# Kernel optimization log

Hardware: AMD Instinct MI355X
Metric: run time of the kernel (lower is better)

The kernel has to match this reference:

```python
import jax, jax.numpy as jnp
import numpy as np

B, S, HID = 2, 2048, 2048
H, KVH, D = 32, 4, 128
EPS = 1e-6
ROPE_THETA = 1e6
INIT = 0.02


def setup_inputs() -> dict:
    key = jax.random.key(0)
    ks = jax.random.split(key, 6)
    hidden_states = jax.random.normal(ks[0], (B, S, HID), jnp.float32)
    q_w = jax.random.normal(ks[1], (HID, H * D), jnp.float32) * INIT
    k_w = jax.random.normal(ks[2], (HID, KVH * D), jnp.float32) * INIT
    v_w = jax.random.normal(ks[3], (HID, KVH * D), jnp.float32) * INIT
    o_w = jax.random.normal(ks[4], (H * D, HID), jnp.float32) * INIT
    q_norm_w = jnp.ones((D,), jnp.float32)
    k_norm_w = jnp.ones((D,), jnp.float32)
    # rotary embeddings, computed once per position (B, S, D)
    pos = jnp.arange(S, dtype=jnp.float32)
    inv_freq = 1.0 / (ROPE_THETA ** (jnp.arange(0, D, 2, dtype=jnp.float32) / D))
    freqs = pos[:, None] * inv_freq[None, :]          # (S, D/2)
    emb = jnp.concatenate([freqs, freqs], axis=-1)    # (S, D)
    cos = jnp.broadcast_to(jnp.cos(emb)[None], (B, S, D))
    sin = jnp.broadcast_to(jnp.sin(emb)[None], (B, S, D))
    # causal mask (is_causal=True, sliding_window=None)
    attn_mask = jnp.tril(jnp.ones((S, S), bool))[None, None]  # (1,1,S,S)
    return {"hidden_states": hidden_states, "cos": cos, "sin": sin,
            "q_w": q_w, "k_w": k_w, "v_w": v_w, "o_w": o_w,
            "q_norm_w": q_norm_w, "k_norm_w": k_norm_w, "attn_mask": attn_mask}


def _rms_norm(x, w):
    xf = x.astype(jnp.float32)
    var = jnp.mean(jax.lax.square(xf), axis=-1, keepdims=True)
    return (w * (xf * jax.lax.rsqrt(var + EPS))).astype(x.dtype)


def _rotate_half(x):
    x1, x2 = jnp.split(x, 2, axis=-1)
    return jnp.concatenate([-x2, x1], axis=-1)


def _apply_rope(q, k, cos, sin):
    # q: (B,H,S,D), k: (B,KVH,S,D); cos/sin: (B,S,D) -> (B,1,S,D)
    cos = cos[:, None]
    sin = sin[:, None]
    q = q * cos + _rotate_half(q) * sin
    k = k * cos + _rotate_half(k) * sin
    return q, k


def reference(hidden_states, cos, sin, q_w, k_w, v_w, o_w, q_norm_w, k_norm_w, attn_mask):
    b, s, _ = hidden_states.shape
    scaling = D ** (-0.5)
    # projections + per-head QK RMSNorm
    q = _rms_norm((hidden_states @ q_w).reshape(b, s, H, D), q_norm_w)
    k = _rms_norm((hidden_states @ k_w).reshape(b, s, KVH, D), k_norm_w)
    v = (hidden_states @ v_w).reshape(b, s, KVH, D)
    q = jnp.transpose(q, (0, 2, 1, 3))   # (b,H,s,D)
    k = jnp.transpose(k, (0, 2, 1, 3))   # (b,KVH,s,D)
    v = jnp.transpose(v, (0, 2, 1, 3))
    q, k = _apply_rope(q, k, cos, sin)
    # GQA: repeat KV heads across groups
    groups = H // KVH
    k = jnp.repeat(k, groups, axis=1)    # (b,H,s,D)
    v = jnp.repeat(v, groups, axis=1)
    # eager softmax attention (fp32 softmax)
    scores = jnp.einsum('bhqd,bhkd->bhqk', q, k).astype(jnp.float32) * scaling
    scores = jnp.where(attn_mask, scores, jnp.float32(-1e30))
    probs = jax.nn.softmax(scores, axis=-1).astype(q.dtype)
    attn = jnp.einsum('bhqk,bhkd->bhqd', probs, v)
    attn = jnp.transpose(attn, (0, 2, 1, 3)).reshape(b, s, H * D)
    return attn @ o_w
```

## Files before the change

kernel.cpp:

```cpp
#include <hip/hip_runtime.h>
#include <hip/hip_bf16.h>

typedef unsigned short u16;
typedef __attribute__((ext_vector_type(4))) float f32x4;
typedef __attribute__((ext_vector_type(16))) float f32x16;
typedef __attribute__((ext_vector_type(8))) short bf16x8;
typedef __attribute__((ext_vector_type(4))) unsigned u32x4;

#define B_ 2
#define S_ 2048
#define HID_ 2048
#define H_ 32
#define KVH_ 4
#define D_ 128
#define M_ 4096
#define NQ_ 4096
#define NKV_ 512

typedef const __attribute__((address_space(1))) void gconst_void;
typedef __attribute__((address_space(3))) void lds_void;

static __device__ __forceinline__ void gload_lds16(const void* g, void* l) {
  __builtin_amdgcn_global_load_lds((gconst_void*)g, (lds_void*)l, 16, 0, 0);
}

#define WAITV(N) asm volatile("s_waitcnt vmcnt(" #N ")" ::: "memory")
#define WAITL0() asm volatile("s_waitcnt lgkmcnt(0)" ::: "memory")
#define SBAR() __builtin_amdgcn_s_barrier()
#define SCHED0() __builtin_amdgcn_sched_barrier(0)
#define CFENCE() asm volatile("" ::: "memory")

static __device__ __forceinline__ u16 f2b(float f) {
  union { float f; unsigned i; } x; x.f = f;
  return (u16)((x.i + 0x7fffu + ((x.i >> 16) & 1u)) >> 16);
}
static __device__ __forceinline__ float b2f(u16 u) {
  union { unsigned i; float f; } x; x.i = ((unsigned)u) << 16;
  return x.f;
}
static __device__ __forceinline__ float max3f(float a, float b, float c) {
  float d;
  asm("v_max3_f32 %0, %1, %2, %3" : "=v"(d) : "v"(a), "v"(b), "v"(c));
  return d;
}

static __device__ __forceinline__ void tr_tile(const float* __restrict__ W,
    u16* __restrict__ Wt, int K, int N, int n0, int k0, u16 (*t)[72]) {
  int tid = threadIdx.x;
  int r = tid >> 4;
  int c4 = (tid & 15) * 4;
#pragma unroll
  for (int i = 0; i < 4; i++) {
    int k = r + i * 16;
    float4 v = *reinterpret_cast<const float4*>(W + (size_t)(k0 + k) * N + n0 + c4);
    t[k][c4 + 0] = f2b(v.x); t[k][c4 + 1] = f2b(v.y);
    t[k][c4 + 2] = f2b(v.z); t[k][c4 + 3] = f2b(v.w);
  }
  __syncthreads();
#pragma unroll
  for (int i = 0; i < 4; i++) {
    int n = r + i * 16;
    ushort4 o;
    o.x = t[c4 + 0][n]; o.y = t[c4 + 1][n]; o.z = t[c4 + 2][n]; o.w = t[c4 + 3][n];
    *reinterpret_cast<ushort4*>(Wt + (size_t)(n0 + n) * K + k0 + c4) = o;
  }
}

__global__ __launch_bounds__(256) void k_prep(const float* __restrict__ hidden, u16* __restrict__ hb,
    const float* __restrict__ qw, u16* __restrict__ qwt,
    const float* __restrict__ kw, u16* __restrict__ kwt,
    const float* __restrict__ vw, u16* __restrict__ vwt,
    const float* __restrict__ ow, u16* __restrict__ owt) {
  __shared__ u16 t[64][72];
  const int bid = blockIdx.x;
  if (bid < 2048) {
    const int n4 = M_ * HID_ / 4;
    int i = bid * 256 + threadIdx.x;
    const int stride = 2048 * 256;
    for (; i < n4; i += stride) {
      float4 v = reinterpret_cast<const float4*>(hidden)[i];
      ushort4 o;
      o.x = f2b(v.x); o.y = f2b(v.y); o.z = f2b(v.z); o.w = f2b(v.w);
      reinterpret_cast<ushort4*>(hb)[i] = o;
    }
  } else if (bid < 4096) {
    int l = bid - 2048;
    tr_tile(qw, qwt, HID_, NQ_, (l & 63) * 64, (l >> 6) * 64, t);
  } else if (bid < 4352) {
    int l = bid - 4096;
    tr_tile(kw, kwt, HID_, NKV_, (l & 7) * 64, (l >> 3) * 64, t);
  } else if (bid < 4608) {
    int l = bid - 4352;
    tr_tile(vw, vwt, HID_, NKV_, (l & 7) * 64, (l >> 3) * 64, t);
  } else {
    int l = bid - 4608;
    tr_tile(ow, owt, NQ_, HID_, (l & 31) * 64, (l >> 5) * 64, t);
  }
}

__device__ __forceinline__ void gemm_core(const u16* __restrict__ A, const u16* __restrict__ Bt,
                                          int K, int m0, int n0,
                                          u16* As, u16* Bs, f32x4 (&acc)[4][4]) {
  const int tid = threadIdx.x;
  const int lane = tid & 63;
  const int wid = tid >> 6;
  const int wr = wid >> 1, wc = wid & 1;
  const int lrow = lane & 15;
  const int hi = lane >> 4;
  const f32x4 zz = {0.f, 0.f, 0.f, 0.f};
#pragma unroll
  for (int i = 0; i < 4; i++)
#pragma unroll
    for (int j = 0; j < 4; j++) acc[i][j] = zz;

  const int srow = tid >> 3;
  const int sc16 = tid & 7;
  const int nk = K >> 6;
  int cur = 0;

#pragma unroll
  for (int rep = 0; rep < 4; rep++) {
    int row = rep * 32 + srow;
    int gcol = ((sc16 ^ (row & 7)) << 3);
    gload_lds16(A + (size_t)(m0 + row) * K + gcol, As + row * 64 + sc16 * 8);
    gload_lds16(Bt + (size_t)(n0 + row) * K + gcol, Bs + row * 64 + sc16 * 8);
  }

  for (int t = 0; t < nk; t++) {
    if (t + 1 < nk) {
      int nxt = cur ^ 1;
      int kb = (t + 1) << 6;
#pragma unroll
      for (int rep = 0; rep < 4; rep++) {
        int row = rep * 32 + srow;
        int gcol = kb + ((sc16 ^ (row & 7)) << 3);
        gload_lds16(A + (size_t)(m0 + row) * K + gcol, As + nxt * 8192 + row * 64 + sc16 * 8);
        gload_lds16(Bt + (size_t)(n0 + row) * K + gcol, Bs + nxt * 8192 + row * 64 + sc16 * 8);
      }
      WAITV(8);
    } else {
      WAITV(0);
    }
    SCHED0(); SBAR(); CFENCE(); SCHED0();

    const u16* Ac = As + cur * 8192;
    const u16* Bc = Bs + cur * 8192;
#pragma unroll
    for (int kc = 0; kc < 2; kc++) {
      bf16x8 af[4], bfr[4];
#pragma unroll
      for (int i = 0; i < 4; i++) {
        int row = wr * 64 + i * 16 + lrow;
        af[i] = *reinterpret_cast<const bf16x8*>(Ac + row * 64 + ((((kc << 2) + hi) ^ (row & 7)) << 3));
      }
#pragma unroll
      for (int j = 0; j < 4; j++) {
        int row = wc * 64 + j * 16 + lrow;
        bfr[j] = *reinterpret_cast<const bf16x8*>(Bc + row * 64 + ((((kc << 2) + hi) ^ (row & 7)) << 3));
      }
#pragma unroll
      for (int i = 0; i < 4; i++)
#pragma unroll
        for (int j = 0; j < 4; j++)
          acc[i][j] = __builtin_amdgcn_mfma_f32_16x16x32_bf16(af[i], bfr[j], acc[i][j], 0, 0, 0);
    }
    SBAR(); SCHED0();
    cur ^= 1;
  }
}

__global__ __launch_bounds__(512, 2) void k_gemm_q8(const u16* __restrict__ A,
    const u16* __restrict__ Bt, u16* __restrict__ qb) {
  __shared__ u16 Ash[2][2][128 * 64];
  __shared__ u16 Bsh[2][2][128 * 64];
  const int bid = blockIdx.x;
  const int wg = (bid & 7) * 32 + (bid >> 3);
  const int mt = wg & 15, nt = wg >> 4;
  const int m0 = mt * 256, n0 = nt * 256;
  const int K = HID_, nk = K >> 6;
  const int tid = threadIdx.x, lane = tid & 63;
  const int wv = tid >> 6, wr = wv >> 2, wc = wv & 3;
  const int lrow = lane & 15, hi4 = lane >> 4;

  const int s0r = tid >> 3, sc = tid & 7;
  const int s1r = (tid + 512) >> 3;

  auto stgA = [&](int h, int t, int d) {
    gload_lds16(A + (size_t)(m0 + h * 128 + s0r) * K + t * 64 + ((sc ^ (s0r & 7)) << 3),
                &Ash[d][h][s0r * 64 + sc * 8]);
    gload_lds16(A + (size_t)(m0 + h * 128 + s1r) * K + t * 64 + ((sc ^ (s1r & 7)) << 3),
                &Ash[d][h][s1r * 64 + sc * 8]);
  };
  auto stgB = [&](int h, int t, int d) {
    gload_lds16(Bt + (size_t)(n0 + h * 128 + s0r) * K + t * 64 + ((sc ^ (s0r & 7)) << 3),
                &Bsh[d][h][s0r * 64 + sc * 8]);
    gload_lds16(Bt + (size_t)(n0 + h * 128 + s1r) * K + t * 64 + ((sc ^ (s1r & 7)) << 3),
                &Bsh[d][h][s1r * 64 + sc * 8]);
  };

  f32x4 acc[8][4];
  const f32x4 zz = {0.f, 0.f, 0.f, 0.f};
#pragma unroll
  for (int f = 0; f < 8; f++)
#pragma unroll
    for (int j = 0; j < 4; j++) acc[f][j] = zz;

  bf16x8 af0[4][2], af1[4][2], bfr[2][2];

  auto lda = [&](bf16x8 (&dst)[4][2], int mh, int d) {
#pragma unroll
    for (int fi = 0; fi < 4; fi++) {
      int row = fi * 32 + wr * 16 + lrow;
#pragma unroll
      for (int kk = 0; kk < 2; kk++)
        dst[fi][kk] = *reinterpret_cast<const bf16x8*>(
            &Ash[d][mh][row * 64 + ((((kk << 2) + hi4) ^ (row & 7)) << 3)]);
    }
  };
  auto ldb = [&](int nh, int d) {
#pragma unroll
    for (int ji = 0; ji < 2; ji++) {
      int row = ji * 64 + wc * 16 + lrow;
#pragma unroll
      for (int kk = 0; kk < 2; kk++)
        bfr[ji][kk] = *reinterpret_cast<const bf16x8*>(
            &Bsh[d][nh][row * 64 + ((((kk << 2) + hi4) ^ (row & 7)) << 3)]);
    }
  };
  auto mq = [&](bf16x8 (&afh)[4][2], int mh, int nh) {
    __builtin_amdgcn_s_setprio(1);
#pragma unroll
    for (int kk = 0; kk < 2; kk++)
#pragma unroll
      for (int fi = 0; fi < 4; fi++)
#pragma unroll
        for (int ji = 0; ji < 2; ji++)
          acc[mh * 4 + fi][nh * 2 + ji] = __builtin_amdgcn_mfma_f32_16x16x32_bf16(
              afh[fi][kk], bfr[ji][kk], acc[mh * 4 + fi][nh * 2 + ji], 0, 0, 0);
    __builtin_amdgcn_s_setprio(0);
  };

  stgA(0, 0, 0); stgA(1, 0, 0); stgB(0, 0, 0); stgB(1, 0, 0);
  WAITV(2); SCHED0();
  SBAR(); SCHED0();

  for (int t = 0; t < nk; t++) {
    const int d = t & 1, nd = d ^ 1;
    const bool pre = (t + 1 < nk);
    lda(af0, 0, d); ldb(0, d);
    if (pre) stgA(0, t + 1, nd);
    SCHED0(); SBAR();
    WAITL0(); SCHED0();
    mq(af0, 0, 0);
    SBAR(); SCHED0();
    lda(af1, 1, d);
    if (pre) stgA(1, t + 1, nd);
    WAITV(4); SCHED0(); SBAR();
    WAITL0(); SCHED0();
    mq(af1, 1, 0);
    SBAR(); SCHED0();
    ldb(1, d);
    if (pre) stgB(0, t + 1, nd);
    SCHED0(); SBAR();
    WAITL0(); SCHED0();
    mq(af1, 1, 1);
    SBAR(); SCHED0();
    if (pre) stgB(1, t + 1, nd);
    WAITV(2); SCHED0(); SBAR();
    mq(af0, 0, 1);
    SBAR(); SCHED0();
  }

  const int lr4 = hi4 * 4, lc = lane & 15;
#pragma unroll
  for (int f = 0; f < 8; f++)
#pragma unroll
    for (int j = 0; j < 4; j++)
#pragma unroll
      for (int rr = 0; rr < 4; rr++) {
        int m = m0 + f * 32 + wr * 16 + lr4 + rr;
        int ncol = n0 + j * 64 + wc * 16 + lc;
        int b = m >> 11, s = m & (S_ - 1);
        int head = ncol >> 7, dd = ncol & 127;
        qb[(((size_t)b * H_ + head) * S_ + s) * D_ + dd] = f2b(acc[f][j][rr]);
      }
}

__global__ __launch_bounds__(256, 2) void k_gemm_kv(const u16* __restrict__ hb,
    const u16* __restrict__ kwt, const u16* __restrict__ vwt,
    u16* __restrict__ kb, u16* __restrict__ vb) {
  __shared__ u16 As[2 * 128 * 64], Bs[2 * 128 * 64];
  const int bid = blockIdx.x;
  const int wg = (bid & 7) * 32 + (bid >> 3);
  const int mt = wg & 31, nt = wg >> 5;
  const bool isv = nt >= 4;
  const int head = isv ? nt - 4 : nt;
  const u16* Bt = isv ? vwt : kwt;
  f32x4 acc[4][4];
  gemm_core(hb, Bt, HID_, mt * 128, head * 128, As, Bs, acc);
  const int lane = threadIdx.x & 63;
  const int wid = threadIdx.x >> 6;
  const int wr = wid >> 1, wc = wid & 1;
  const int lr4 = (lane >> 4) * 4, lc = lane & 15;
#pragma unroll
  for (int i = 0; i < 4; i++)
#pragma unroll
    for (int j = 0; j < 4; j++)
#pragma unroll
      for (int r = 0; r < 4; r++) {
        int m = mt * 128 + wr * 64 + i * 16 + lr4 + r;
        int d = wc * 64 + j * 16 + lc;
        int b = m >> 11, s = m & (S_ - 1);
        u16 val = f2b(acc[i][j][r]);
        if (isv) vb[(((size_t)b * KVH_ + head) * D_ + d) * S_ + s] = val;
        else     kb[(((size_t)b * KVH_ + head) * S_ + s) * D_ + d] = val;
      }
}

__global__ __launch_bounds__(256, 2) void k_gemm_o(const u16* __restrict__ ab,
    const u16* __restrict__ owt, float* __restrict__ out) {
  __shared__ u16 As[2 * 128 * 64], Bs[2 * 128 * 64];
  const int bid = blockIdx.x;
  const int wg = (bid & 7) * 64 + (bid >> 3);
  const int mt = wg & 31, nt = wg >> 5;
  f32x4 acc[4][4];
  gemm_core(ab, owt, NQ_, mt * 128, nt * 128, As, Bs, acc);
  const int lane = threadIdx.x & 63;
  const int wid = threadIdx.x >> 6;
  const int wr = wid >> 1, wc = wid & 1;
  const int lr4 = (lane >> 4) * 4, lc = lane & 15;
#pragma unroll
  for (int i = 0; i < 4; i++)
#pragma unroll
    for (int j = 0; j < 4; j++)
#pragma unroll
      for (int r = 0; r < 4; r++) {
        int m = mt * 128 + wr * 64 + i * 16 + lr4 + r;
        int n = nt * 128 + wc * 64 + j * 16 + lc;
        out[(size_t)m * HID_ + n] = acc[i][j][r];
      }
}

__global__ __launch_bounds__(256) void k_norm_rope(u16* __restrict__ qb, u16* __restrict__ kb,
    const float* __restrict__ cosp, const float* __restrict__ sinp,
    const float* __restrict__ qnw, const float* __restrict__ knw) {
  int row = blockIdx.x * 4 + (threadIdx.x >> 6);
  int lane = threadIdx.x & 63;
  const int QROWS = B_ * H_ * S_;
  u16* ptr; const float* nw; int b, s; float os;
  if (row < QROWS) {
    ptr = qb + (size_t)row * D_; nw = qnw;
    s = row & (S_ - 1); b = row / (H_ * S_);
    os = 0.08838834764831845f * 1.44269504088896340f;
  } else {
    int r2 = row - QROWS;
    ptr = kb + (size_t)r2 * D_; nw = knw;
    s = r2 & (S_ - 1); b = r2 / (KVH_ * S_);
    os = 1.0f;
  }
  int d = lane * 2;
  float x0 = b2f(ptr[d]), x1 = b2f(ptr[d + 1]);
  float ss = x0 * x0 + x1 * x1;
#pragma unroll
  for (int m = 1; m < 64; m <<= 1) ss += __shfl_xor(ss, m);
  float inv = rsqrtf(ss * (1.0f / 128.0f) + 1e-6f) * os;
  x0 = x0 * inv * nw[d]; x1 = x1 * inv * nw[d + 1];
  float p0 = __shfl_xor(x0, 32), p1 = __shfl_xor(x1, 32);
  float r0 = (lane < 32) ? -p0 : p0;
  float r1 = (lane < 32) ? -p1 : p1;
  const float* cp = cosp + ((size_t)b * S_ + s) * D_;
  const float* sp = sinp + ((size_t)b * S_ + s) * D_;
  ptr[d]     = f2b(x0 * cp[d]     + r0 * sp[d]);
  ptr[d + 1] = f2b(x1 * cp[d + 1] + r1 * sp[d + 1]);
}

__global__ __launch_bounds__(512, 2) void k_attn(const u16* __restrict__ q,
    const u16* __restrict__ k, const u16* __restrict__ vt, u16* __restrict__ out) {
  __shared__ u16 Kb[2 * 64 * 128];
  __shared__ u16 Vb[2 * 128 * 64];
  const int bid = blockIdx.x;
  const int wg = (bid & 7) * 32 + (bid >> 3);
  const int qx = wg & 3, bh = wg >> 2;
  const int b = bh >> 5, h = bh & 31;
  const int kvh = h >> 3;
  const int tid = threadIdx.x, lane = tid & 63, w = tid >> 6;
  const int lq = lane & 31, hi = lane >> 5;
  const u16* qp  = q  + ((size_t)(b * H_ + h) * S_) * D_;
  const u16* kp  = k  + ((size_t)(b * KVH_ + kvh) * S_) * D_;
  const u16* vtp = vt + ((size_t)(b * KVH_ + kvh) * D_) * S_;

  const int rowKa = tid >> 4;
  const int colK  = ((tid & 15) ^ (rowKa & 15)) << 3;
  const int rowVa = tid >> 3;
  const int colV  = ((tid & 7) ^ (rowVa & 7)) << 3;

  const f32x16 z16 = {0.f};
  int cur = 0;

  for (int half = 0; half < 2; half++) {
    const int qt = half ? (7 - qx) : qx;
    const int q0 = qt * 256;
    const int last = 4 * qt + 3;
    const int qg = q0 + 32 * w + lq;

    {
      u16* kd = Kb + cur * 8192 + tid * 8;
      u16* vd = Vb + cur * 8192 + tid * 8;
      gload_lds16(kp + (size_t)rowKa * D_ + colK, kd);
      gload_lds16(kp + (size_t)(rowKa + 32) * D_ + colK, kd + 4096);
      gload_lds16(vtp + (size_t)rowVa * S_ + colV, vd);
      gload_lds16(vtp + (size_t)(rowVa + 64) * S_ + colV, vd + 4096);
    }

    bf16x8 qf[8];
#pragma unroll
    for (int ds = 0; ds < 8; ds++)
      qf[ds] = *reinterpret_cast<const bf16x8*>(qp + (size_t)qg * D_ + ds * 16 + hi * 8);

    f32x16 oacc[4];
#pragma unroll
    for (int dt = 0; dt < 4; dt++) oacc[dt] = z16;
    float mrun = -1e30f, lrun = 0.f;

    for (int nt = 0; nt <= last; nt++) {
      const int n0 = nt * 64;
      if (nt < last) {
        const int n1 = n0 + 64;
        u16* kd = Kb + (cur ^ 1) * 8192 + tid * 8;
        u16* vd = Vb + (cur ^ 1) * 8192 + tid * 8;
        gload_lds16(kp + (size_t)(n1 + rowKa) * D_ + colK, kd);
        gload_lds16(kp + (size_t)(n1 + rowKa + 32) * D_ + colK, kd + 4096);
        gload_lds16(vtp + (size_t)rowVa * S_ + n1 + colV, vd);
        gload_lds16(vtp + (size_t)(rowVa + 64) * S_ + n1 + colV, vd + 4096);
        WAITV(4);
      } else {
        WAITV(0);
      }
      SCHED0(); SBAR(); CFENCE(); SCHED0();

      const u16* Kc = Kb + cur * 8192;
      const u16* Vc = Vb + cur * 8192;

      const bool skip = (n0 > q0 + 32 * w + 31);
      if (!skip) {
        const bool needmask = (n0 + 63 > q0 + 32 * w);

        f32x16 sacc[2];
        sacc[0] = z16; sacc[1] = z16;
#pragma unroll
        for (int ds = 0; ds < 8; ds++) {
          const int sl = (((ds << 1) + hi) ^ (lq & 15)) << 3;
          bf16x8 ka0 = *reinterpret_cast<const bf16x8*>(Kc + lq * 128 + sl);
          bf16x8 ka1 = *reinterpret_cast<const bf16x8*>(Kc + (lq + 32) * 128 + sl);
          __builtin_amdgcn_s_setprio(1);
          sacc[0] = __builtin_amdgcn_mfma_f32_32x32x16_bf16(ka0, qf[ds], sacc[0], 0, 0, 0);
          sacc[1] = __builtin_amdgcn_mfma_f32_32x32x16_bf16(ka1, qf[ds], sacc[1], 0, 0, 0);
          __builtin_amdgcn_s_setprio(0);
        }

        if (needmask) {
#pragma unroll
          for (int t = 0; t < 2; t++)
#pragma unroll
            for (int r = 0; r < 16; r++) {
              int kvg = n0 + 32 * t + (r & 3) + 8 * (r >> 2) + 4 * hi;
              if (kvg > qg) sacc[t][r] = -1e30f;
            }
        }
        float tm = fmaxf(sacc[0][0], sacc[0][1]);
#pragma unroll
        for (int i = 1; i < 16; i++) {
          const int e0 = 2 * i, e1 = 2 * i + 1;
          tm = max3f(tm, sacc[e0 >> 4][e0 & 15], sacc[e1 >> 4][e1 & 15]);
        }
        tm = fmaxf(tm, __shfl_xor(tm, 32));
        if (__any(tm > mrun + 8.f)) {
          float mn = fmaxf(mrun, tm);
          float al = exp2f(mrun - mn);
          mrun = mn;
          lrun *= al;
#pragma unroll
          for (int r = 0; r < 16; r++) {
            float ar = __shfl(al, (r & 3) + 8 * (r >> 2) + 4 * hi);
#pragma unroll
            for (int dt = 0; dt < 4; dt++) oacc[dt][r] *= ar;
          }
        }
        float rs = 0.f;
#pragma unroll
        for (int t = 0; t < 2; t++)
#pragma unroll
          for (int r = 0; r < 16; r++) {
            float pv = exp2f(sacc[t][r] - mrun);
            sacc[t][r] = pv;
            rs += pv;
          }
        rs += __shfl_xor(rs, 32);
        lrun += rs;

        u32x4 pa[4];
#pragma unroll
        for (int t = 0; t < 2; t++)
#pragma unroll
          for (int ksl = 0; ksl < 2; ksl++) {
            unsigned wa, wb, wc2, wd;
            asm("v_cvt_pk_bf16_f32 %0, %1, %2" : "=v"(wa)
                : "v"(sacc[t][8 * ksl + 0]), "v"(sacc[t][8 * ksl + 1]));
            asm("v_cvt_pk_bf16_f32 %0, %1, %2" : "=v"(wb)
                : "v"(sacc[t][8 * ksl + 2]), "v"(sacc[t][8 * ksl + 3]));
            asm("v_cvt_pk_bf16_f32 %0, %1, %2" : "=v"(wc2)
                : "v"(sacc[t][8 * ksl + 4]), "v"(sacc[t][8 * ksl + 5]));
            asm("v_cvt_pk_bf16_f32 %0, %1, %2" : "=v"(wd)
                : "v"(sacc[t][8 * ksl + 6]), "v"(sacc[t][8 * ksl + 7]));
            asm("v_permlane32_swap_b32 %0, %1" : "+v"(wa), "+v"(wc2));
            asm("v_permlane32_swap_b32 %0, %1" : "+v"(wb), "+v"(wd));
            u32x4 t4 = {wa, wb, wc2, wd};
            pa[t * 2 + ksl] = t4;
          }

#pragma unroll
        for (int ks = 0; ks < 4; ks++) {
          bf16x8 paf = __builtin_bit_cast(bf16x8, pa[ks]);
          bf16x8 bv[4];
#pragma unroll
          for (int dt = 0; dt < 4; dt++) {
            int rowv = dt * 32 + lq;
            bv[dt] = *reinterpret_cast<const bf16x8*>(
                Vc + rowv * 64 + ((((ks << 1) + hi) ^ (rowv & 7)) << 3));
          }
          __builtin_amdgcn_s_setprio(1);
#pragma unroll
          for (int dt = 0; dt < 4; dt++)
            oacc[dt] = __builtin_amdgcn_mfma_f32_32x32x16_bf16(paf, bv[dt], oacc[dt], 0, 0, 0);
          __builtin_amdgcn_s_setprio(0);
        }
      }
      SBAR(); SCHED0();
      cur ^= 1;
    }

    float linv = 1.0f / lrun;
#pragma unroll
    for (int r = 0; r < 16; r++) {
      const int idx_r = (r & 3) + 8 * (r >> 2) + 4 * hi;
      float lr = __shfl(linv, idx_r);
      size_t base = ((size_t)b * S_ + (q0 + 32 * w + idx_r)) * NQ_ + h * D_ + lq;
#pragma unroll
      for (int dt = 0; dt < 4; dt++)
        out[base + dt * 32] = f2b(oacc[dt][r] * lr);
    }
  }
}

extern "C" void kernel_launch(void* const* d_in, const int* in_sizes, int n_in,
                              void* d_out, int out_size, void* d_ws, size_t ws_size,
                              hipStream_t stream) {
  const float* hidden = (const float*)d_in[0];
  const float* cosp   = (const float*)d_in[1];
  const float* sinp   = (const float*)d_in[2];
  const float* q_w    = (const float*)d_in[3];
  const float* k_w    = (const float*)d_in[4];
  const float* v_w    = (const float*)d_in[5];
  const float* o_w    = (const float*)d_in[6];
  const float* qnw    = (const float*)d_in[7];
  const float* knw    = (const float*)d_in[8];

  char* p = (char*)d_ws;
  u16* hb  = (u16*)p; p += (size_t)M_ * HID_ * 2;
  u16* qwt = (u16*)p; p += (size_t)NQ_ * HID_ * 2;
  u16* kwt = (u16*)p; p += (size_t)NKV_ * HID_ * 2;
  u16* vwt = (u16*)p; p += (size_t)NKV_ * HID_ * 2;
  u16* owt = (u16*)p; p += (size_t)HID_ * NQ_ * 2;
  u16* qb  = (u16*)p; p += (size_t)B_ * H_ * S_ * D_ * 2;
  u16* kb  = (u16*)p; p += (size_t)B_ * KVH_ * S_ * D_ * 2;
  u16* vb  = (u16*)p; p += (size_t)B_ * KVH_ * S_ * D_ * 2;
  u16* ab  = (u16*)p; p += (size_t)M_ * NQ_ * 2;

  k_prep<<<6656, 256, 0, stream>>>(hidden, hb, q_w, qwt, k_w, kwt, v_w, vwt, o_w, owt);
  k_gemm_q8<<<256, 512, 0, stream>>>(hb, qwt, qb);
  k_gemm_kv<<<256, 256, 0, stream>>>(hb, kwt, vwt, kb, vb);
  k_norm_rope<<<(B_ * H_ * S_ + B_ * KVH_ * S_) / 4, 256, 0, stream>>>(qb, kb, cosp, sinp, qnw, knw);
  k_attn<<<256, 512, 0, stream>>>(qb, kb, vb, ab);
  k_gemm_o<<<512, 256, 0, stream>>>(ab, owt, (float*)d_out);
}
```

Before: 336.6 us.

## Split attention KV loop across two warp-groups with split-K merge

The attention kernel now runs 1024 threads per block as two 512-thread groups that each process 18 KV tiles in parallel. Group 1 finishes part of the high query tile's KV range, spills its partial output and max/sum stats to scratch, then switches to the low query tile. Group 0 merges the partial softmax state when it finishes. This shortens the serial KV chain per block and balances the causal work. In exchange it adds scratch traffic, reuses the weight-workspace buffers as scratch, and stores the partial output in bf16, which costs some precision.

New measurement: 527.1 us. +56.6%, slower.

```diff
diff --git a/kernel.cpp b/kernel.cpp
--- a/kernel.cpp
+++ b/kernel.cpp
@@ -374,177 +374,239 @@
   ptr[d + 1] = f2b(x1 * cp[d + 1] + r1 * sp[d + 1]);
 }
 
-__global__ __launch_bounds__(512, 2) void k_attn(const u16* __restrict__ q,
-    const u16* __restrict__ k, const u16* __restrict__ vt, u16* __restrict__ out) {
-  __shared__ u16 Kb[2 * 64 * 128];
-  __shared__ u16 Vb[2 * 128 * 64];
+__global__ __launch_bounds__(1024, 1) void k_attn(const u16* __restrict__ q,
+    const u16* __restrict__ k, const u16* __restrict__ vt, u16* __restrict__ out,
+    u16* __restrict__ scrO, float* __restrict__ scrML) {
+  __shared__ u16 Kb[2 * 2 * 64 * 128];
+  __shared__ u16 Vb[2 * 2 * 128 * 64];
   const int bid = blockIdx.x;
-  const int wg = (bid & 7) * 32 + (bid >> 3);
-  const int qx = wg & 3, bh = wg >> 2;
+  const int wgid = (bid & 7) * 32 + (bid >> 3);
+  const int qx = wgid & 3, bh = wgid >> 2;
   const int b = bh >> 5, h = bh & 31;
   const int kvh = h >> 3;
-  const int tid = threadIdx.x, lane = tid & 63, w = tid >> 6;
+  const int tid = threadIdx.x;
+  const int g = tid >> 9;
+  const int gtid = tid & 511;
+  const int lane = tid & 63, w = gtid >> 6;
   const int lq = lane & 31, hi = lane >> 5;
   const u16* qp  = q  + ((size_t)(b * H_ + h) * S_) * D_;
   const u16* kp  = k  + ((size_t)(b * KVH_ + kvh) * S_) * D_;
   const u16* vtp = vt + ((size_t)(b * KVH_ + kvh) * D_) * S_;
 
-  const int rowKa = tid >> 4;
-  const int colK  = ((tid & 15) ^ (rowKa & 15)) << 3;
-  const int rowVa = tid >> 3;
-  const int colV  = ((tid & 7) ^ (rowVa & 7)) << 3;
+  const int Nh = 32 - 4 * qx;
+  const int sB = Nh - 18;
+  const int q0h = (7 - qx) * 256;
+  const int q0l = qx * 256;
+
+  const int rowKa = gtid >> 4;
+  const int colK  = ((gtid & 15) ^ (rowKa & 15)) << 3;
+  const int rowVa = gtid >> 3;
+  const int colV  = ((gtid & 7) ^ (rowVa & 7)) << 3;
+  u16* KG = Kb + g * 16384;
+  u16* VG = Vb + g * 16384;
+
+  auto nmap = [&](int i) { return (g == 0) ? i : ((i < sB) ? 18 + i : i - sB); };
+  auto stage = [&](int n, int cu) {
+    u16* kd = KG + cu * 8192 + gtid * 8;
+    u16* vd = VG + cu * 8192 + gtid * 8;
+    const u16* ks = kp + (size_t)(n * 64 + rowKa) * D_ + colK;
+    gload_lds16(ks, kd);
+    gload_lds16(ks + 32 * D_, kd + 4096);
+    const u16* vs = vtp + (size_t)rowVa * S_ + n * 64 + colV;
+    gload_lds16(vs, vd);
+    gload_lds16(vs + (size_t)64 * S_, vd + 4096);
+  };
 
   const f32x16 z16 = {0.f};
+  int q0 = q0h;
+  bf16x8 qf[8];
+#pragma unroll
+  for (int ds = 0; ds < 8; ds++)
+    qf[ds] = *reinterpret_cast<const bf16x8*>(qp + (size_t)(q0 + 32 * w + lq) * D_ + ds * 16 + hi * 8);
+
+  f32x16 oacc[4];
+#pragma unroll
+  for (int dt = 0; dt < 4; dt++) oacc[dt] = z16;
+  float mrun = -1e30f, lrun = 0.f;
+
+  stage(nmap(0), 0);
   int cur = 0;
 
-  for (int half = 0; half < 2; half++) {
-    const int qt = half ? (7 - qx) : qx;
-    const int q0 = qt * 256;
-    const int last = 4 * qt + 3;
+  for (int i = 0; i < 18; i++) {
+    if (i < 17) {
+      stage(nmap(i + 1), cur ^ 1);
+      WAITV(4);
+    } else {
+      WAITV(0);
+    }
+    SCHED0(); SBAR(); CFENCE(); SCHED0();
+
+    if (g == 1 && i == sB) {
+      unsigned* o32 = (unsigned*)scrO + (size_t)bid * 16384;
+#pragma unroll
+      for (int dt = 0; dt < 4; dt++)
+#pragma unroll
+        for (int r = 0; r < 16; r += 2) {
+          unsigned pk;
+          asm("v_cvt_pk_bf16_f32 %0, %1, %2" : "=v"(pk)
+              : "v"(oacc[dt][r]), "v"(oacc[dt][r + 1]));
+          int rowb = 32 * w + (r & 3) + 8 * (r >> 2) + 4 * hi;
+          o32[(dt * 32 + lq) * 128 + (rowb >> 1)] = pk;
+        }
+      if (hi == 0) {
+        scrML[(size_t)bid * 512 + 32 * w + lq] = mrun;
+        scrML[(size_t)bid * 512 + 256 + 32 * w + lq] = lrun;
+      }
+#pragma unroll
+      for (int dt = 0; dt < 4; dt++) oacc[dt] = z16;
+      mrun = -1e30f; lrun = 0.f;
+      q0 = q0l;
+#pragma unroll
+      for (int ds = 0; ds < 8; ds++)
+        qf[ds] = *reinterpret_cast<const bf16x8*>(
+            qp + (size_t)(q0 + 32 * w + lq) * D_ + ds * 16 + hi * 8);
+    }
+
+    const int n0 = nmap(i) * 64;
     const int qg = q0 + 32 * w + lq;
-
-    {
-      u16* kd = Kb + cur * 8192 + tid * 8;
-      u16* vd = Vb + cur * 8192 + tid * 8;
-      gload_lds16(kp + (size_t)rowKa * D_ + colK, kd);
-      gload_lds16(kp + (size_t)(rowKa + 32) * D_ + colK, kd + 4096);
-      gload_lds16(vtp + (size_t)rowVa * S_ + colV, vd);
-      gload_lds16(vtp + (size_t)(rowVa + 64) * S_ + colV, vd + 4096);
-    }
-
-    bf16x8 qf[8];
-#pragma unroll
-    for (int ds = 0; ds < 8; ds++)
-      qf[ds] = *reinterpret_cast<const bf16x8*>(qp + (size_t)qg * D_ + ds * 16 + hi * 8);
-
-    f32x16 oacc[4];
-#pragma unroll
-    for (int dt = 0; dt < 4; dt++) oacc[dt] = z16;
-    float mrun = -1e30f, lrun = 0.f;
-
-    for (int nt = 0; nt <= last; nt++) {
-      const int n0 = nt * 64;
-      if (nt < last) {
-        const int n1 = n0 + 64;
-        u16* kd = Kb + (cur ^ 1) * 8192 + tid * 8;
-        u16* vd = Vb + (cur ^ 1) * 8192 + tid * 8;
-        gload_lds16(kp + (size_t)(n1 + rowKa) * D_ + colK, kd);
-        gload_lds16(kp + (size_t)(n1 + rowKa + 32) * D_ + colK, kd + 4096);
-        gload_lds16(vtp + (size_t)rowVa * S_ + n1 + colV, vd);
-        gload_lds16(vtp + (size_t)(rowVa + 64) * S_ + n1 + colV, vd + 4096);
-        WAITV(4);
-      } else {
-        WAITV(0);
-      }
-      SCHED0(); SBAR(); CFENCE(); SCHED0();
-
-      const u16* Kc = Kb + cur * 8192;
-      const u16* Vc = Vb + cur * 8192;
-
-      const bool skip = (n0 > q0 + 32 * w + 31);
-      if (!skip) {
-        const bool needmask = (n0 + 63 > q0 + 32 * w);
-
-        f32x16 sacc[2];
-        sacc[0] = z16; sacc[1] = z16;
-#pragma unroll
-        for (int ds = 0; ds < 8; ds++) {
-          const int sl = (((ds << 1) + hi) ^ (lq & 15)) << 3;
-          bf16x8 ka0 = *reinterpret_cast<const bf16x8*>(Kc + lq * 128 + sl);
-          bf16x8 ka1 = *reinterpret_cast<const bf16x8*>(Kc + (lq + 32) * 128 + sl);
-          __builtin_amdgcn_s_setprio(1);
-          sacc[0] = __builtin_amdgcn_mfma_f32_32x32x16_bf16(ka0, qf[ds], sacc[0], 0, 0, 0);
-          sacc[1] = __builtin_amdgcn_mfma_f32_32x32x16_bf16(ka1, qf[ds], sacc[1], 0, 0, 0);
-          __builtin_amdgcn_s_setprio(0);
+    const u16* Kc = KG + cur * 8192;
+    const u16* Vc = VG + cur * 8192;
+
+    const bool skip = (n0 > q0 + 32 * w + 31);
+    if (!skip) {
+      const bool needmask = (n0 + 63 > q0 + 32 * w);
+
+      f32x16 sacc[2];
+      sacc[0] = z16; sacc[1] = z16;
+#pragma unroll
+      for (int ds = 0; ds < 8; ds++) {
+        const int sl = (((ds << 1) + hi) ^ (lq & 15)) << 3;
+        bf16x8 ka0 = *reinterpret_cast<const bf16x8*>(Kc + lq * 128 + sl);
+        bf16x8 ka1 = *reinterpret_cast<const bf16x8*>(Kc + (lq + 32) * 128 + sl);
+        __builtin_amdgcn_s_setprio(1);
+        sacc[0] = __builtin_amdgcn_mfma_f32_32x32x16_bf16(ka0, qf[ds], sacc[0], 0, 0, 0);
+        sacc[1] = __builtin_amdgcn_mfma_f32_32x32x16_bf16(ka1, qf[ds], sacc[1], 0, 0, 0);
+        __builtin_amdgcn_s_setprio(0);
+      }
+
+      if (needmask) {
+#pragma unroll
+        for (int t = 0; t < 2; t++)
+#pragma unroll
+          for (int r = 0; r < 16; r++) {
+            int kvg = n0 + 32 * t + (r & 3) + 8 * (r >> 2) + 4 * hi;
+            if (kvg > qg) sacc[t][r] = -1e30f;
+          }
+      }
+      float tm = fmaxf(sacc[0][0], sacc[0][1]);
+#pragma unroll
+      for (int i2 = 1; i2 < 16; i2++) {
+        const int e0 = 2 * i2, e1 = 2 * i2 + 1;
+        tm = max3f(tm, sacc[e0 >> 4][e0 & 15], sacc[e1 >> 4][e1 & 15]);
+      }
+      tm = fmaxf(tm, __shfl_xor(tm, 32));
+      if (__any(tm > mrun + 8.f)) {
+        float mn = fmaxf(mrun, tm);
+        float al = exp2f(mrun - mn);
+        mrun = mn;
+        lrun *= al;
+#pragma unroll
+        for (int r = 0; r < 16; r++) {
+          float ar = __shfl(al, (r & 3) + 8 * (r >> 2) + 4 * hi);
+#pragma unroll
+          for (int dt = 0; dt < 4; dt++) oacc[dt][r] *= ar;
         }
-
-        if (needmask) {
-#pragma unroll
-          for (int t = 0; t < 2; t++)
-#pragma unroll
-            for (int r = 0; r < 16; r++) {
-              int kvg = n0 + 32 * t + (r & 3) + 8 * (r >> 2) + 4 * hi;
-              if (kvg > qg) sacc[t][r] = -1e30f;
-            }
+      }
+      float rs = 0.f;
+#pragma unroll
+      for (int t = 0; t < 2; t++)
+#pragma unroll
+        for (int r = 0; r < 16; r++) {
+          float pv = exp2f(sacc[t][r] - mrun);
+          sacc[t][r] = pv;
+          rs += pv;
         }
-        float tm = fmaxf(sacc[0][0], sacc[0][1]);
-#pragma unroll
-        for (int i = 1; i < 16; i++) {
-          const int e0 = 2 * i, e1 = 2 * i + 1;
-          tm = max3f(tm, sacc[e0 >> 4][e0 & 15], sacc[e1 >> 4][e1 & 15]);
+      rs += __shfl_xor(rs, 32);
+      lrun += rs;
+
+      u32x4 pa[4];
+#pragma unroll
+      for (int t = 0; t < 2; t++)
+#pragma unroll
+        for (int ksl = 0; ksl < 2; ksl++) {
+          unsigned wa, wb, wc2, wd;
+          asm("v_cvt_pk_bf16_f32 %0, %1, %2" : "=v"(wa)
+              : "v"(sacc[t][8 * ksl + 0]), "v"(sacc[t][8 * ksl + 1]));
+          asm("v_cvt_pk_bf16_f32 %0, %1, %2" : "=v"(wb)
+              : "v"(sacc[t][8 * ksl + 2]), "v"(sacc[t][8 * ksl + 3]));
+          asm("v_cvt_pk_bf16_f32 %0, %1, %2" : "=v"(wc2)
+              : "v"(sacc[t][8 * ksl + 4]), "v"(sacc[t][8 * ksl + 5]));
+          asm("v_cvt_pk_bf16_f32 %0, %1, %2" : "=v"(wd)
+              : "v"(sacc[t][8 * ksl + 6]), "v"(sacc[t][8 * ksl + 7]));
+          asm("v_permlane32_swap_b32 %0, %1" : "+v"(wa), "+v"(wc2));
+          asm("v_permlane32_swap_b32 %0, %1" : "+v"(wb), "+v"(wd));
+          u32x4 t4 = {wa, wb, wc2, wd};
+          pa[t * 2 + ksl] = t4;
         }
-        tm = fmaxf(tm, __shfl_xor(tm, 32));
-        if (__any(tm > mrun + 8.f)) {
-          float mn = fmaxf(mrun, tm);
-          float al = exp2f(mrun - mn);
-          mrun = mn;
-          lrun *= al;
-#pragma unroll
-          for (int r = 0; r < 16; r++) {
-            float ar = __shfl(al, (r & 3) + 8 * (r >> 2) + 4 * hi);
-#pragma unroll
-            for (int dt = 0; dt < 4; dt++) oacc[dt][r] *= ar;
-          }
+
+#pragma unroll
+      for (int ks = 0; ks < 4; ks++) {
+        bf16x8 paf = __builtin_bit_cast(bf16x8, pa[ks]);
+        bf16x8 bv[4];
+#pragma unroll
+        for (int dt = 0; dt < 4; dt++) {
+          int rowv = dt * 32 + lq;
+          bv[dt] = *reinterpret_cast<const bf16x8*>(
+              Vc + rowv * 64 + ((((ks << 1) + hi) ^ (rowv & 7)) << 3));
         }
-        float rs = 0.f;
-#pragma unroll
-        for (int t = 0; t < 2; t++)
-#pragma unroll
-          for (int r = 0; r < 16; r++) {
-            float pv = exp2f(sacc[t][r] - mrun);
-            sacc[t][r] = pv;
-            rs += pv;
-          }
-        rs += __shfl_xor(rs, 32);
-        lrun += rs;
-
-        u32x4 pa[4];
-#pragma unroll
-        for (int t = 0; t < 2; t++)
-#pragma unroll
-          for (int ksl = 0; ksl < 2; ksl++) {
-            unsigned wa, wb, wc2, wd;
-            asm("v_cvt_pk_bf16_f32 %0, %1, %2" : "=v"(wa)
-                : "v"(sacc[t][8 * ksl + 0]), "v"(sacc[t][8 * ksl + 1]));
-            asm("v_cvt_pk_bf16_f32 %0, %1, %2" : "=v"(wb)
-                : "v"(sacc[t][8 * ksl + 2]), "v"(sacc[t][8 * ksl + 3]));
-            asm("v_cvt_pk_bf16_f32 %0, %1, %2" : "=v"(wc2)
-                : "v"(sacc[t][8 * ksl + 4]), "v"(sacc[t][8 * ksl + 5]));
-            asm("v_cvt_pk_bf16_f32 %0, %1, %2" : "=v"(wd)
-                : "v"(sacc[t][8 * ksl + 6]), "v"(sacc[t][8 * ksl + 7]));
-            asm("v_permlane32_swap_b32 %0, %1" : "+v"(wa), "+v"(wc2));
-            asm("v_permlane32_swap_b32 %0, %1" : "+v"(wb), "+v"(wd));
-            u32x4 t4 = {wa, wb, wc2, wd};
-            pa[t * 2 + ksl] = t4;
-          }
-
-#pragma unroll
-        for (int ks = 0; ks < 4; ks++) {
-          bf16x8 paf = __builtin_bit_cast(bf16x8, pa[ks]);
-          bf16x8 bv[4];
-#pragma unroll
-          for (int dt = 0; dt < 4; dt++) {
-            int rowv = dt * 32 + lq;
-            bv[dt] = *reinterpret_cast<const bf16x8*>(
-                Vc + rowv * 64 + ((((ks << 1) + hi) ^ (rowv & 7)) << 3));
-          }
-          __builtin_amdgcn_s_setprio(1);
-#pragma unroll
-          for (int dt = 0; dt < 4; dt++)
-            oacc[dt] = __builtin_amdgcn_mfma_f32_32x32x16_bf16(paf, bv[dt], oacc[dt], 0, 0, 0);
-          __builtin_amdgcn_s_setprio(0);
-        }
-      }
-      SBAR(); SCHED0();
-      cur ^= 1;
-    }
-
+        __builtin_amdgcn_s_setprio(1);
+#pragma unroll
+        for (int dt = 0; dt < 4; dt++)
+          oacc[dt] = __builtin_amdgcn_mfma_f32_32x32x16_bf16(paf, bv[dt], oacc[dt], 0, 0, 0);
+        __builtin_amdgcn_s_setprio(0);
+      }
+    }
+    SBAR(); SCHED0();
+    cur ^= 1;
+  }
+
+  if (g == 0) {
+    const unsigned* o32 = (const unsigned*)scrO + (size_t)bid * 16384;
+    float sA[16], sBv[16], li[16];
+#pragma unroll
+    for (int r = 0; r < 16; r++) {
+      int riw = (r & 3) + 8 * (r >> 2) + 4 * hi;
+      int row = 32 * w + riw;
+      float mb = scrML[(size_t)bid * 512 + row];
+      float lb = scrML[(size_t)bid * 512 + 256 + row];
+      float ma = __shfl(mrun, riw);
+      float la = __shfl(lrun, riw);
+      float m = fmaxf(ma, mb);
+      float aA = exp2f(ma - m), aB = exp2f(mb - m);
+      sA[r] = aA; sBv[r] = aB;
+      li[r] = 1.0f / (la * aA + lb * aB);
+    }
+#pragma unroll
+    for (int dt = 0; dt < 4; dt++)
+#pragma unroll
+      for (int r = 0; r < 16; r += 2) {
+        int rowb = 32 * w + (r & 3) + 8 * (r >> 2) + 4 * hi;
+        unsigned pk = o32[(dt * 32 + lq) * 128 + (rowb >> 1)];
+        float ob0 = b2f((u16)(pk & 0xffffu));
+        float ob1 = b2f((u16)(pk >> 16));
+        float v0 = (oacc[dt][r] * sA[r] + ob0 * sBv[r]) * li[r];
+        float v1 = (oacc[dt][r + 1] * sA[r + 1] + ob1 * sBv[r + 1]) * li[r + 1];
+        size_t base = ((size_t)b * S_ + (q0h + rowb)) * NQ_ + h * D_ + dt * 32 + lq;
+        out[base] = f2b(v0);
+        out[base + NQ_] = f2b(v1);
+      }
+  } else {
     float linv = 1.0f / lrun;
 #pragma unroll
     for (int r = 0; r < 16; r++) {
       const int idx_r = (r & 3) + 8 * (r >> 2) + 4 * hi;
       float lr = __shfl(linv, idx_r);
-      size_t base = ((size_t)b * S_ + (q0 + 32 * w + idx_r)) * NQ_ + h * D_ + lq;
+      size_t base = ((size_t)b * S_ + (q0l + 32 * w + idx_r)) * NQ_ + h * D_ + lq;
 #pragma unroll
       for (int dt = 0; dt < 4; dt++)
         out[base + dt * 32] = f2b(oacc[dt][r] * lr);
@@ -580,6 +642,6 @@
   k_gemm_q8<<<256, 512, 0, stream>>>(hb, qwt, qb);
   k_gemm_kv<<<256, 256, 0, stream>>>(hb, kwt, vwt, kb, vb);
   k_norm_rope<<<(B_ * H_ * S_ + B_ * KVH_ * S_) / 4, 256, 0, stream>>>(qb, kb, cosp, sinp, qnw, knw);
-  k_attn<<<256, 512, 0, stream>>>(qb, kb, vb, ab);
+  k_attn<<<256, 1024, 0, stream>>>(qb, kb, vb, ab, qwt, (float*)kwt);
   k_gemm_o<<<512, 256, 0, stream>>>(ab, owt, (float*)d_out);
 }
```
